# Optimization experiments

Measured on AMD Instinct MI355X. Metric: run time of the kernel, lower is better.

Reference implementation:

```python
import jax, jax.numpy as jnp
import numpy as np

DEFAULT_MASK_VALUE = -0.7 * float(np.finfo(np.float32).max)


def setup_inputs() -> dict:
    key = jax.random.key(0)
    kq, kk, kv = jax.random.split(key, 3)
    B, S, Hq, Hkv, D = 2, 2048, 16, 8, 128
    return {
        "query": jax.random.normal(kq, (B, S, Hq, D), dtype=jnp.float32),
        "key": jax.random.normal(kk, (B, S, Hkv, D), dtype=jnp.float32),
        "value": jax.random.normal(kv, (B, S, Hkv, D), dtype=jnp.float32),
        "chunk_size": 512,
    }


def reference(query, key, value, chunk_size):
    """Chunked-causal GQA attention (AttentionOp with attention_type='chunk').

    Tokens attend only within their own chunk, causally. This is exactly the
    mask from _generate_chunk_attention_mask, exploited as a block-diagonal
    structure so cross-chunk logits are never materialized.
    """
    B, S, Hq, D = query.shape
    Hkv = key.shape[2]
    G = Hq // Hkv  # GQA group size
    C = int(chunk_size)
    NC = S // C
    scale = 1.0 / np.float32(np.sqrt(D))  # depth scaling (folded into query init in MaxText)

    # float32 qk product / logits (float32_qk_product & float32_logits = True)
    qf = query.astype(jnp.float32).reshape(B, NC, C, Hkv, G, D)
    kf = key.astype(jnp.float32).reshape(B, NC, C, Hkv, D)
    vf = value.reshape(B, NC, C, Hkv, D)

    # per-chunk logits: [B, NC, Hkv, G, C(q), C(k)]
    logits = jnp.einsum("bnqhgd,bnkhd->bnhgqk", qf, kf) * scale

    # causal mask within each chunk (apply_mask_to_logits semantics)
    causal = jnp.arange(C)[:, None] >= jnp.arange(C)[None, :]
    logits = jnp.where(causal, logits, DEFAULT_MASK_VALUE)

    probs = jax.nn.softmax(logits, axis=-1).astype(value.dtype)
    out = jnp.einsum("bnhgqk,bnkhd->bnqhgd", probs, vf)
    return out.reshape(B, S, Hq, D)
```

## Files before the change

### kernel.cpp

```cpp
#include <hip/hip_runtime.h>
#include <hip/hip_bf16.h>

typedef __bf16 bf16;
typedef bf16  bf16x2 __attribute__((ext_vector_type(2)));
typedef bf16  bf16x4 __attribute__((ext_vector_type(4)));
typedef bf16  bf16x8 __attribute__((ext_vector_type(8)));
typedef float f32x4  __attribute__((ext_vector_type(4)));
typedef float f32x16 __attribute__((ext_vector_type(16)));

#define MFMA32(A, B, C) __builtin_amdgcn_mfma_f32_32x32x16_bf16((A), (B), (C), 0, 0, 0)

namespace {
constexpr int   kS = 2048, kHq = 16, kHkv = 8, kD = 128, kChunk = 512;
constexpr int   kStrK  = kHkv * kD;
constexpr float kLog2e = 1.4426950408889634f;
constexpr float kScale = 0.08838834764831845f * kLog2e;
constexpr float kThr   = 8.0f * kLog2e;
}

union U32B { bf16x2 h; unsigned u; };
union PAU  { unsigned u[4]; bf16x8 v; };

__device__ __forceinline__ void lgkm_barrier() {
  __builtin_amdgcn_sched_barrier(0);
  asm volatile("s_waitcnt lgkmcnt(0)" ::: "memory");
  __builtin_amdgcn_s_barrier();
  __builtin_amdgcn_sched_barrier(0);
}

__global__ __launch_bounds__(512, 2)
void attn_chunk(const float* __restrict__ Qg, const float* __restrict__ Kg,
                const float* __restrict__ Vg, float* __restrict__ Og) {
  __shared__ __attribute__((aligned(16))) bf16 ldsK[4][64 * 128];
  __shared__ __attribute__((aligned(16))) bf16 ldsV[4][128 * 64];

  const int t = threadIdx.x, lane = t & 63, w = t >> 6;
  const int l31 = lane & 31, hi = lane >> 5;

  const int bid = blockIdx.x;
  const int gid = (bid & 7) * 32 + (bid >> 3);
  const int p = gid & 1, hq = (gid >> 1) & 15, n = (gid >> 5) & 3, b = (gid >> 7) & 1;
  const int h = hq >> 1;

  const int a      = (w < 4) ? (7 - 2 * w) : (2 * w - 8);
  const int need   = a + 1;
  const int strip  = 2 * a + p;
  const int qg     = n * kChunk + strip * 32 + l31;
  const int rowoff = 32 * p + l31;

  bf16x8 qf[8];
  {
    const float* qp = Qg + ((size_t)(b * kS + qg) * kHq + hq) * kD;
#pragma unroll
    for (int dk = 0; dk < 8; ++dk) {
      f32x4 x0 = *(const f32x4*)(qp + dk * 16 + 8 * hi);
      f32x4 x1 = *(const f32x4*)(qp + dk * 16 + 8 * hi + 4);
      bf16x8 v;
#pragma unroll
      for (int q = 0; q < 4; ++q) { v[q] = (bf16)(x0[q] * kScale); v[4 + q] = (bf16)(x1[q] * kScale); }
      qf[dk] = v;
    }
  }

  f32x16 o[4];
#pragma unroll
  for (int dt = 0; dt < 4; ++dt)
#pragma unroll
    for (int r = 0; r < 16; ++r) o[dt][r] = 0.f;
  float m = -1e30f, l = 0.f;

  const float* kpz = Kg + ((size_t)(b * kS + n * kChunk) * kHkv + h) * kD;
  const float* vpz = Vg + ((size_t)(b * kS + n * kChunk) * kHkv + h) * kD;

  const int sKey = t >> 5, sD4 = t & 31;
  const int vKp = t & 31, vD4h = t >> 5;

  f32x4 kf[4], va[2], vb[2];
  auto issue = [&](int kt) {
    const float* kp = kpz + (size_t)kt * 64 * kStrK;
    const float* vp = vpz + (size_t)kt * 64 * kStrK;
#pragma unroll
    for (int it = 0; it < 4; ++it)
      kf[it] = *(const f32x4*)(kp + (size_t)(16 * it + sKey) * kStrK + sD4 * 4);
#pragma unroll
    for (int it = 0; it < 2; ++it) {
      va[it] = *(const f32x4*)(vp + (size_t)(2 * vKp) * kStrK + (16 * it + vD4h) * 4);
      vb[it] = *(const f32x4*)(vp + (size_t)(2 * vKp + 1) * kStrK + (16 * it + vD4h) * 4);
    }
  };
  auto stage = [&](int buf) {
#pragma unroll
    for (int it = 0; it < 4; ++it) {
      const int key = 16 * it + sKey;
      bf16x4 kb;
#pragma unroll
      for (int q = 0; q < 4; ++q) kb[q] = (bf16)kf[it][q];
      *(bf16x4*)&ldsK[buf][key * 128 + ((sD4 * 4) ^ ((key & 7) << 3))] = kb;
    }
#pragma unroll
    for (int it = 0; it < 2; ++it) {
#pragma unroll
      for (int q = 0; q < 4; ++q) {
        const int d = (16 * it + vD4h) * 4 + q;
        U32B uu; uu.h = bf16x2{(bf16)va[it][q], (bf16)vb[it][q]};
        *(unsigned*)&ldsV[buf][d * 64 + ((2 * vKp) ^ ((d & 7) << 3))] = uu.u;
      }
    }
  };

  auto compute = [&](int buf, bool diag) {
    f32x16 s[2];
#pragma unroll
    for (int ks = 0; ks < 2; ++ks)
#pragma unroll
      for (int r = 0; r < 16; ++r) s[ks][r] = 0.f;
    __builtin_amdgcn_s_setprio(1);
#pragma unroll
    for (int ks = 0; ks < 2; ++ks) {
      const int key = ks * 32 + l31, swz = (key & 7) << 3;
      const bf16* kb = &ldsK[buf][key * 128];
#pragma unroll
      for (int dk = 0; dk < 8; ++dk) {
        bf16x8 kfr = *(const bf16x8*)&kb[(dk * 16 + 8 * hi) ^ swz];
        s[ks] = MFMA32(kfr, qf[dk], s[ks]);
      }
    }
    __builtin_amdgcn_s_setprio(0);
    if (diag) {
#pragma unroll
      for (int ks = 0; ks < 2; ++ks)
#pragma unroll
        for (int r = 0; r < 16; ++r) {
          const int key = ks * 32 + (r & 3) + 8 * (r >> 2) + 4 * hi;
          if (key > rowoff) s[ks][r] = -1e30f;
        }
    }
    float mx = -1e30f;
#pragma unroll
    for (int ks = 0; ks < 2; ++ks)
#pragma unroll
      for (int r = 0; r < 16; ++r) mx = fmaxf(mx, s[ks][r]);
    mx = fmaxf(mx, __shfl_xor(mx, 32, 64));
    if (__any(mx > m + kThr)) {
      const float mn = fmaxf(m, mx), c = exp2f(m - mn);
      l *= c;
#pragma unroll
      for (int dt = 0; dt < 4; ++dt)
#pragma unroll
        for (int r = 0; r < 16; ++r) o[dt][r] *= c;
      m = mn;
    }
    unsigned u[2][8];
    float lp = 0.f;
#pragma unroll
    for (int ks = 0; ks < 2; ++ks)
#pragma unroll
      for (int q = 0; q < 8; ++q) {
        const float p0 = exp2f(s[ks][2 * q] - m), p1 = exp2f(s[ks][2 * q + 1] - m);
        lp += p0 + p1;
        U32B uu; uu.h = bf16x2{(bf16)p0, (bf16)p1};
        u[ks][q] = uu.u;
      }
    l += lp;
    unsigned rc[2][4];
#pragma unroll
    for (int ks = 0; ks < 2; ++ks)
#pragma unroll
      for (int i = 0; i < 4; ++i)
        rc[ks][i] = (unsigned)__shfl_xor((int)u[ks][(i & 1) + 4 * (i >> 1) + (hi ? 0 : 2)], 32, 64);
    bf16x8 pa[4];
#pragma unroll
    for (int ks = 0; ks < 2; ++ks)
#pragma unroll
      for (int kh = 0; kh < 2; ++kh) {
        PAU pu;
        pu.u[0] = hi ? rc[ks][2 * kh]     : u[ks][4 * kh];
        pu.u[1] = hi ? rc[ks][2 * kh + 1] : u[ks][4 * kh + 1];
        pu.u[2] = hi ? u[ks][4 * kh + 2]  : rc[ks][2 * kh];
        pu.u[3] = hi ? u[ks][4 * kh + 3]  : rc[ks][2 * kh + 1];
        pa[ks * 2 + kh] = pu.v;
      }
    __builtin_amdgcn_s_setprio(1);
#pragma unroll
    for (int dt = 0; dt < 4; ++dt) {
      const int d = dt * 32 + l31, swz = (d & 7) << 3;
      const bf16* vbp = &ldsV[buf][d * 64];
#pragma unroll
      for (int ksl = 0; ksl < 4; ++ksl) {
        bf16x8 vfr = *(const bf16x8*)&vbp[(ksl * 16 + 8 * hi) ^ swz];
        o[dt] = MFMA32(vfr, pa[ksl], o[dt]);
      }
    }
    __builtin_amdgcn_s_setprio(0);
  };

  issue(0);
  stage(0);
  issue(1);
  stage(1);
  issue(2);
  lgkm_barrier();
#pragma unroll 1
  for (int i = 0; i < 8; ++i) {
    if (i < need) compute(i & 3, i + 1 == need);
    if (i + 2 < 8) stage((i + 2) & 3);
    if (i + 3 < 8) issue(i + 3);
    if ((i & 1) == 1 && i < 7) lgkm_barrier();
  }

  l += __shfl_xor(l, 32, 64);
  const float inv = 1.f / l;
  float* op = Og + ((size_t)(b * kS + qg) * kHq + hq) * kD;
#pragma unroll
  for (int dt = 0; dt < 4; ++dt)
#pragma unroll
    for (int rq = 0; rq < 4; ++rq) {
      f32x4 st;
#pragma unroll
      for (int rr = 0; rr < 4; ++rr) st[rr] = o[dt][4 * rq + rr] * inv;
      *(f32x4*)(op + dt * 32 + 8 * rq + 4 * hi) = st;
    }
}

extern "C" void kernel_launch(void* const* d_in, const int* in_sizes, int n_in,
                              void* d_out, int out_size, void* d_ws, size_t ws_size,
                              hipStream_t stream) {
  (void)in_sizes; (void)n_in; (void)d_ws; (void)ws_size; (void)out_size;
  const float* Q = (const float*)d_in[0];
  const float* K = (const float*)d_in[1];
  const float* V = (const float*)d_in[2];
  float* O = (float*)d_out;
  dim3 grid(256);
  dim3 block(512);
  hipLaunchKernelGGL(attn_chunk, grid, block, 0, stream, Q, K, V, O);
}
```

Measured before the change: 36.39 us.

## Prepack K/V to swizzled bf16 tiles and stream them via global_load_lds

```diff
diff --git a/kernel.cpp b/kernel.cpp
--- a/kernel.cpp
+++ b/kernel.cpp
@@ -16,23 +16,85 @@
 constexpr float kLog2e = 1.4426950408889634f;
 constexpr float kScale = 0.08838834764831845f * kLog2e;
 constexpr float kThr   = 8.0f * kLog2e;
+constexpr size_t kWsNeed = 2ull * 512 * 8192 * sizeof(bf16);
 }
 
 union U32B { bf16x2 h; unsigned u; };
 union PAU  { unsigned u[4]; bf16x8 v; };
 
-__device__ __forceinline__ void lgkm_barrier() {
+__device__ __forceinline__ void glds16(const bf16* g, bf16* l) {
+  __builtin_amdgcn_global_load_lds(
+      (const __attribute__((address_space(1))) unsigned*)g,
+      (__attribute__((address_space(3))) unsigned*)l, 16, 0, 0);
+}
+__device__ __forceinline__ void bar() {
   __builtin_amdgcn_sched_barrier(0);
-  asm volatile("s_waitcnt lgkmcnt(0)" ::: "memory");
   __builtin_amdgcn_s_barrier();
   __builtin_amdgcn_sched_barrier(0);
 }
+#define VMWAIT(n)                                          \
+  do {                                                     \
+    __builtin_amdgcn_sched_barrier(0);                     \
+    asm volatile("s_waitcnt vmcnt(" #n ")" ::: "memory");  \
+    __builtin_amdgcn_sched_barrier(0);                     \
+  } while (0)
+
+__global__ __launch_bounds__(256, 4)
+void prepack(const float* __restrict__ Kg, const float* __restrict__ Vg,
+             bf16* __restrict__ Kws, bf16* __restrict__ Vws) {
+  __shared__ __attribute__((aligned(16))) bf16 img[8192];
+  const int t  = threadIdx.x;
+  const int bk = blockIdx.x;
+  const int kt = bk & 7, h = (bk >> 3) & 7, n = (bk >> 6) & 3, b = bk >> 8;
+  const size_t rowbase = ((size_t)(b * kS + n * kChunk + kt * 64) * kHkv + h) * kD;
+
+  const float* kp = Kg + rowbase;
+#pragma unroll
+  for (int it = 0; it < 8; ++it) {
+    const int idx = it * 256 + t, key = idx >> 5, d4 = idx & 31;
+    f32x4 v = *(const f32x4*)(kp + (size_t)key * kStrK + d4 * 4);
+    bf16x4 kb;
+#pragma unroll
+    for (int j = 0; j < 4; ++j) kb[j] = (bf16)v[j];
+    *(bf16x4*)&img[key * 128 + ((d4 * 4) ^ ((key & 7) << 3))] = kb;
+  }
+  __syncthreads();
+  {
+    bf16* dst = Kws + (size_t)bk * 8192;
+#pragma unroll
+    for (int i = 0; i < 4; ++i)
+      *(bf16x8*)(dst + t * 8 + i * 2048) = *(const bf16x8*)(&img[t * 8 + i * 2048]);
+  }
+  __syncthreads();
+
+  const float* vp = Vg + rowbase;
+  const int vKp = t & 31, vD4h = t >> 5;
+#pragma unroll
+  for (int it = 0; it < 4; ++it) {
+    const int d4 = 8 * it + vD4h;
+    f32x4 va = *(const f32x4*)(vp + (size_t)(2 * vKp) * kStrK + d4 * 4);
+    f32x4 vb = *(const f32x4*)(vp + (size_t)(2 * vKp + 1) * kStrK + d4 * 4);
+#pragma unroll
+    for (int j = 0; j < 4; ++j) {
+      const int d = d4 * 4 + j;
+      U32B uu; uu.h = bf16x2{(bf16)va[j], (bf16)vb[j]};
+      *(unsigned*)&img[d * 64 + ((2 * vKp) ^ ((d & 7) << 3))] = uu.u;
+    }
+  }
+  __syncthreads();
+  {
+    bf16* dst = Vws + (size_t)bk * 8192;
+#pragma unroll
+    for (int i = 0; i < 4; ++i)
+      *(bf16x8*)(dst + t * 8 + i * 2048) = *(const bf16x8*)(&img[t * 8 + i * 2048]);
+  }
+}
 
 __global__ __launch_bounds__(512, 2)
-void attn_chunk(const float* __restrict__ Qg, const float* __restrict__ Kg,
-                const float* __restrict__ Vg, float* __restrict__ Og) {
-  __shared__ __attribute__((aligned(16))) bf16 ldsK[4][64 * 128];
-  __shared__ __attribute__((aligned(16))) bf16 ldsV[4][128 * 64];
+void attn_main(const float* __restrict__ Qg, const bf16* __restrict__ Kws,
+               const bf16* __restrict__ Vws, float* __restrict__ Og) {
+  __shared__ __attribute__((aligned(16))) bf16 ldsK[2][8192];
+  __shared__ __attribute__((aligned(16))) bf16 ldsV[2][8192];
 
   const int t = threadIdx.x, lane = t & 63, w = t >> 6;
   const int l31 = lane & 31, hi = lane >> 5;
@@ -69,42 +131,15 @@
     for (int r = 0; r < 16; ++r) o[dt][r] = 0.f;
   float m = -1e30f, l = 0.f;
 
-  const float* kpz = Kg + ((size_t)(b * kS + n * kChunk) * kHkv + h) * kD;
-  const float* vpz = Vg + ((size_t)(b * kS + n * kChunk) * kHkv + h) * kD;
-
-  const int sKey = t >> 5, sD4 = t & 31;
-  const int vKp = t & 31, vD4h = t >> 5;
-
-  f32x4 kf[4], va[2], vb[2];
-  auto issue = [&](int kt) {
-    const float* kp = kpz + (size_t)kt * 64 * kStrK;
-    const float* vp = vpz + (size_t)kt * 64 * kStrK;
-#pragma unroll
-    for (int it = 0; it < 4; ++it)
-      kf[it] = *(const f32x4*)(kp + (size_t)(16 * it + sKey) * kStrK + sD4 * 4);
-#pragma unroll
-    for (int it = 0; it < 2; ++it) {
-      va[it] = *(const f32x4*)(vp + (size_t)(2 * vKp) * kStrK + (16 * it + vD4h) * 4);
-      vb[it] = *(const f32x4*)(vp + (size_t)(2 * vKp + 1) * kStrK + (16 * it + vD4h) * 4);
-    }
-  };
-  auto stage = [&](int buf) {
-#pragma unroll
-    for (int it = 0; it < 4; ++it) {
-      const int key = 16 * it + sKey;
-      bf16x4 kb;
-#pragma unroll
-      for (int q = 0; q < 4; ++q) kb[q] = (bf16)kf[it][q];
-      *(bf16x4*)&ldsK[buf][key * 128 + ((sD4 * 4) ^ ((key & 7) << 3))] = kb;
-    }
-#pragma unroll
-    for (int it = 0; it < 2; ++it) {
-#pragma unroll
-      for (int q = 0; q < 4; ++q) {
-        const int d = (16 * it + vD4h) * 4 + q;
-        U32B uu; uu.h = bf16x2{(bf16)va[it][q], (bf16)vb[it][q]};
-        *(unsigned*)&ldsV[buf][d * 64 + ((2 * vKp) ^ ((d & 7) << 3))] = uu.u;
-      }
+  const int tbase = ((b * 4 + n) * 8 + h) * 8;
+  auto issueT = [&](int kt, int buf) {
+    const bf16* kb = Kws + (size_t)(tbase + kt) * 8192;
+    const bf16* vb = Vws + (size_t)(tbase + kt) * 8192;
+#pragma unroll
+    for (int c = 0; c < 2; ++c) {
+      const int chunk = 2 * w + c;
+      glds16(kb + chunk * 512 + lane * 8, &ldsK[buf][chunk * 512]);
+      glds16(vb + chunk * 512 + lane * 8, &ldsV[buf][chunk * 512]);
     }
   };
 
@@ -194,18 +229,23 @@
     __builtin_amdgcn_s_setprio(0);
   };
 
-  issue(0);
-  stage(0);
-  issue(1);
-  stage(1);
-  issue(2);
-  lgkm_barrier();
+  issueT(0, 0);
+  issueT(1, 1);
+  VMWAIT(4);
+  bar();
 #pragma unroll 1
-  for (int i = 0; i < 8; ++i) {
-    if (i < need) compute(i & 3, i + 1 == need);
-    if (i + 2 < 8) stage((i + 2) & 3);
-    if (i + 3 < 8) issue(i + 3);
-    if ((i & 1) == 1 && i < 7) lgkm_barrier();
+  for (int kt = 0; kt < 8; ++kt) {
+    if (kt < need) compute(kt & 1, kt + 1 == need);
+    if (kt + 1 < 8) {
+      bar();
+      if (kt + 2 < 8) {
+        issueT(kt + 2, kt & 1);
+        VMWAIT(4);
+      } else {
+        VMWAIT(0);
+      }
+      bar();
+    }
   }
 
   l += __shfl_xor(l, 32, 64);
@@ -225,12 +265,13 @@
 extern "C" void kernel_launch(void* const* d_in, const int* in_sizes, int n_in,
                               void* d_out, int out_size, void* d_ws, size_t ws_size,
                               hipStream_t stream) {
-  (void)in_sizes; (void)n_in; (void)d_ws; (void)ws_size; (void)out_size;
+  (void)in_sizes; (void)n_in; (void)out_size; (void)ws_size;
   const float* Q = (const float*)d_in[0];
   const float* K = (const float*)d_in[1];
   const float* V = (const float*)d_in[2];
   float* O = (float*)d_out;
-  dim3 grid(256);
-  dim3 block(512);
-  hipLaunchKernelGGL(attn_chunk, grid, block, 0, stream, Q, K, V, O);
-}
+  bf16* Kws = (bf16*)d_ws;
+  bf16* Vws = Kws + 512ull * 8192;
+  hipLaunchKernelGGL(prepack, dim3(512), dim3(256), 0, stream, K, V, Kws, Vws);
+  hipLaunchKernelGGL(attn_main, dim3(256), dim3(512), 0, stream, Q, Kws, Vws, O);
+}
```

After: 46.89 us, median of 2. 1.29x slower.
